# Kernel optimization log

Measured on AMD Instinct MI355X. Metric: run time of the kernel, lower is better.

Reference implementation:

```python
import jax, jax.numpy as jnp
import numpy as np

N = 50000          # num nodes
E = 800000         # num edges (avg degree 16)
IN_C, HID_C, OUT_C = 128, 128, 64
LPA_ITER = 5


def setup_inputs() -> dict:
    key = jax.random.key(0)
    ks = jax.random.split(key, 8)
    x = jax.random.normal(ks[0], (N, IN_C), dtype=jnp.float32)
    soft_labels = jax.random.uniform(ks[1], (N, OUT_C), dtype=jnp.float32)
    edge_index = jax.random.randint(ks[2], (2, E), 0, N, dtype=jnp.int64)
    # learnable edge weights: abs() in the original, so keep them positive
    edge_attr = jax.random.uniform(ks[3], (E,), dtype=jnp.float32, minval=0.1, maxval=1.0)
    # GCNConv params (lin weight + bias)
    w1 = jax.random.normal(ks[4], (IN_C, HID_C), dtype=jnp.float32) / np.sqrt(IN_C)
    b1 = jnp.zeros((HID_C,), dtype=jnp.float32)
    w2 = jax.random.normal(ks[5], (HID_C, OUT_C), dtype=jnp.float32) / np.sqrt(HID_C)
    b2 = jnp.zeros((OUT_C,), dtype=jnp.float32)
    return {"x": x, "soft_labels": soft_labels, "edge_attr": edge_attr,
            "w1": w1, "b1": b1, "w2": w2, "b2": b2, "edge_index": edge_index}


def reference(x, soft_labels, edge_attr, w1, b1, w2, b2, edge_index):
    row, col = edge_index[0], edge_index[1]
    n = x.shape[0]
    # row-normalize the weighted sparse adjacency: A_n = D^{-1} A
    deg = jax.ops.segment_sum(edge_attr, row, num_segments=n)  # [N]
    deg_inv = jnp.where(deg == 0, 0.0, 1.0 / deg)              # inf -> 0
    val = deg_inv[row] * edge_attr                              # [E]

    def spmm(v):  # A_n @ v,  v: [N, F]
        return jax.ops.segment_sum(val[:, None] * v[col], row, num_segments=n)

    # eval mode: dropout(p=0.5, training=False) is identity
    h = jax.nn.relu(spmm(x @ w1) + b1)        # GCNConv 1 (normalize=False)
    logits = spmm(h @ w2) + b2                # GCNConv 2
    x_out = jax.nn.sigmoid(logits)

    labels = soft_labels
    for _ in range(LPA_ITER):                 # label propagation
        labels = spmm(labels)
    labels = jax.nn.sigmoid(labels)
    return (x_out, labels)
```

## Files before the change

### kernel.cpp

```cpp
#include <hip/hip_runtime.h>
#include <cstdint>
#include <cstddef>


#define WS_ALIGN(x) (((x) + 255) & ~((size_t)255))

typedef __attribute__((ext_vector_type(8))) short short8;
typedef __attribute__((ext_vector_type(4))) float floatx4;

__device__ __forceinline__ unsigned short f2bf(float f) {
    unsigned u = __float_as_uint(f);
    u += 0x7fffu + ((u >> 16) & 1u);
    return (unsigned short)(u >> 16);
}
__device__ __forceinline__ float bf2f(unsigned short h) {
    return __uint_as_float(((unsigned)h) << 16);
}
__device__ __forceinline__ float sigmoidf(float x) {
    return 1.f / (1.f + __expf(-x));
}

static const int NBLK = 256;
#define MAXNB 256

__launch_bounds__(256)
__global__ void binA_count(const int* __restrict__ row, int* __restrict__ bucket_count,
                           int* __restrict__ bases, int E, int chunk, int NB)
{
    __shared__ int hist[MAXNB];
    const int t = threadIdx.x;
    const int blk = blockIdx.x;
    if (t < NB) hist[t] = 0;
    __syncthreads();
    const int s = blk * chunk;
    const int e = min(E, s + chunk);
    for (int i = s + t; i < e; i += 256)
        atomicAdd(&hist[row[i] >> 8], 1);
    __syncthreads();
    if (t < NB)
        bases[blk * NB + t] = atomicAdd(&bucket_count[t], hist[t]);
}

__launch_bounds__(256)
__global__ void bin_scan(const int* __restrict__ bucket_count, int* __restrict__ bucket_start,
                         int NB)
{
    __shared__ int s[256];
    const int t = threadIdx.x;
    int v = (t < NB) ? bucket_count[t] : 0;
    s[t] = v;
    __syncthreads();
    for (int off = 1; off < 256; off <<= 1) {
        int u = (t >= off) ? s[t - off] : 0;
        __syncthreads();
        s[t] += u;
        __syncthreads();
    }
    int excl = s[t] - v;
    if (t <= NB) bucket_start[t] = excl;
}

__launch_bounds__(256)
__global__ void binA_scatter(const int* __restrict__ row, const int* __restrict__ colv,
                             const float* __restrict__ ea,
                             const int* __restrict__ bucket_start, const int* __restrict__ bases,
                             int2* __restrict__ bk, int E, int chunk, int NB)
{
    __shared__ int cur[MAXNB];
    const int t = threadIdx.x;
    const int blk = blockIdx.x;
    if (t < NB) cur[t] = bucket_start[t] + bases[blk * NB + t];
    __syncthreads();
    const int s = blk * chunk;
    const int e = min(E, s + chunk);
    for (int i = s + t; i < e; i += 256) {
        int r = row[i];
        int bin = r >> 8;
        int pos = atomicAdd(&cur[bin], 1);
        bk[pos] = make_int2(((r & 255) << 16) | colv[i], __float_as_int(ea[i]));
    }
}

__launch_bounds__(256)
__global__ void binB(const int2* __restrict__ bk, const int* __restrict__ bucket_start,
                     int* __restrict__ rowptr, int2* __restrict__ edges, int N)
{
    __shared__ int cnt[256];
    __shared__ float deg[256];
    __shared__ float inv[256];
    __shared__ int excl_s[256];
    __shared__ int cur[256];
    __shared__ int scantmp[256];
    const int b = blockIdx.x;
    const int t = threadIdx.x;
    const int s = bucket_start[b];
    const int e = bucket_start[b + 1];
    cnt[t] = 0;
    deg[t] = 0.f;
    __syncthreads();
    for (int i = s + t; i < e; i += 256) {
        int2 v = bk[i];
        int rl = ((unsigned)v.x) >> 16;
        atomicAdd(&cnt[rl], 1);
        atomicAdd(&deg[rl], __int_as_float(v.y));
    }
    __syncthreads();
    const int myc = cnt[t];
    scantmp[t] = myc;
    __syncthreads();
    for (int off = 1; off < 256; off <<= 1) {
        int u = (t >= off) ? scantmp[t - off] : 0;
        __syncthreads();
        scantmp[t] += u;
        __syncthreads();
    }
    const int excl = scantmp[t] - myc;
    excl_s[t] = excl;
    float d = deg[t];
    inv[t] = (d > 0.f) ? 1.f / d : 0.f;
    cur[t] = 0;
    const int gr = b * 256 + t;
    if (gr <= N) rowptr[gr] = s + excl;
    __syncthreads();
    for (int i = s + t; i < e; i += 256) {
        int2 v = bk[i];
        int rl = ((unsigned)v.x) >> 16;
        int c = v.x & 0xffff;
        int p = s + excl_s[rl] + atomicAdd(&cur[rl], 1);
        edges[p] = make_int2(c, __float_as_int(__int_as_float(v.y) * inv[rl]));
    }
}

__global__ void f32_to_bf16_kernel(const float* __restrict__ in, unsigned short* __restrict__ out,
                                   int n2)
{
    int i = blockIdx.x * 256 + threadIdx.x;
    if (i < n2) {
        float2 v = ((const float2*)in)[i];
        unsigned p = (unsigned)f2bf(v.x) | ((unsigned)f2bf(v.y) << 16);
        ((unsigned*)out)[i] = p;
    }
}

template<int COLS>
__global__ void pack_w_kernel(const float* __restrict__ W, unsigned short* __restrict__ Wp)
{
    const int total = (COLS / 16) * 4 * 64;
    int idx = blockIdx.x * 256 + threadIdx.x;
    if (idx >= total) return;
    const int l = idx & 63;
    const int t = (idx >> 6) & 3;
    const int ct = idx >> 8;
    const int kbase = t * 32 + (l >> 4) * 8;
    const int col = ct * 16 + (l & 15);
    unsigned short v[8];
#pragma unroll
    for (int j = 0; j < 8; ++j)
        v[j] = f2bf(W[(size_t)(kbase + j) * COLS + col]);
    uint4 o;
    o.x = (unsigned)v[0] | ((unsigned)v[1] << 16);
    o.y = (unsigned)v[2] | ((unsigned)v[3] << 16);
    o.z = (unsigned)v[4] | ((unsigned)v[5] << 16);
    o.w = (unsigned)v[6] | ((unsigned)v[7] << 16);
    *(uint4*)(Wp + (size_t)idx * 8) = o;
}

template<int COLS>
__launch_bounds__(256)
__global__ void gemm_mfma(const unsigned short* __restrict__ A,
                          const unsigned short* __restrict__ Wp,
                          unsigned short* __restrict__ C, int M)
{
    const int wave = threadIdx.x >> 6;
    const int lane = threadIdx.x & 63;
    const int row0 = blockIdx.x * 64 + wave * 16;
    const int m = lane & 15;
    const int q = lane >> 4;

    const int arow = row0 + m;
    const bool avalid = arow < M;
    short8 a[4];
#pragma unroll
    for (int t = 0; t < 4; ++t) {
        if (avalid)
            a[t] = *(const short8*)(A + (size_t)arow * 128 + t * 32 + q * 8);
        else
            a[t] = (short8)0;
    }

#pragma unroll
    for (int ct = 0; ct < COLS / 16; ++ct) {
        floatx4 acc = {0.f, 0.f, 0.f, 0.f};
#pragma unroll
        for (int t = 0; t < 4; ++t) {
            short8 b = *(const short8*)(Wp + (size_t)((ct * 4 + t) * 64 + lane) * 8);
            acc = __builtin_amdgcn_mfma_f32_16x16x32_bf16(a[t], b, acc, 0, 0, 0);
        }
        const int col = ct * 16 + m;
#pragma unroll
        for (int r = 0; r < 4; ++r) {
            int orow = row0 + q * 4 + r;
            if (orow < M)
                C[(size_t)orow * COLS + col] = f2bf(acc[r]);
        }
    }
}

__launch_bounds__(256)
__global__ void spmm128_relu(const int* __restrict__ rowptr, const int2* __restrict__ edges,
                             const unsigned short* __restrict__ src,
                             const float* __restrict__ bias, unsigned* __restrict__ out, int n)
{
    const int row = blockIdx.x * 4 + (threadIdx.x >> 6);
    const int lane = threadIdx.x & 63;
    if (row >= n) return;
    const int s = rowptr[row];
    const int e = rowptr[row + 1];
    const unsigned* us = (const unsigned*)src;

    float ax[8], ay[8];
#pragma unroll
    for (int j = 0; j < 8; ++j) { ax[j] = 0.f; ay[j] = 0.f; }
    int i = s;
    for (; i + 8 <= e; i += 8) {
        int2 ed[8];
        unsigned u[8];
#pragma unroll
        for (int j = 0; j < 8; ++j) ed[j] = edges[i + j];
#pragma unroll
        for (int j = 0; j < 8; ++j) u[j] = us[(size_t)ed[j].x * 64 + lane];
#pragma unroll
        for (int j = 0; j < 8; ++j) {
            float w = __int_as_float(ed[j].y);
            ax[j] = fmaf(w, __uint_as_float(u[j] << 16), ax[j]);
            ay[j] = fmaf(w, __uint_as_float(u[j] & 0xffff0000u), ay[j]);
        }
    }
    for (; i + 4 <= e; i += 4) {
        int2 ed[4];
        unsigned u[4];
#pragma unroll
        for (int j = 0; j < 4; ++j) ed[j] = edges[i + j];
#pragma unroll
        for (int j = 0; j < 4; ++j) u[j] = us[(size_t)ed[j].x * 64 + lane];
#pragma unroll
        for (int j = 0; j < 4; ++j) {
            float w = __int_as_float(ed[j].y);
            ax[j] = fmaf(w, __uint_as_float(u[j] << 16), ax[j]);
            ay[j] = fmaf(w, __uint_as_float(u[j] & 0xffff0000u), ay[j]);
        }
    }
    for (; i < e; ++i) {
        int2 e0 = edges[i];
        unsigned u0 = us[(size_t)e0.x * 64 + lane];
        float w0 = __int_as_float(e0.y);
        ax[0] = fmaf(w0, __uint_as_float(u0 << 16), ax[0]);
        ay[0] = fmaf(w0, __uint_as_float(u0 & 0xffff0000u), ay[0]);
    }
    float vx = ((ax[0] + ax[1]) + (ax[2] + ax[3])) + ((ax[4] + ax[5]) + (ax[6] + ax[7]));
    float vy = ((ay[0] + ay[1]) + (ay[2] + ay[3])) + ((ay[4] + ay[5]) + (ay[6] + ay[7]));
    float2 b = *(const float2*)(bias + lane * 2);
    vx = fmaxf(vx + b.x, 0.f);
    vy = fmaxf(vy + b.y, 0.f);
    out[(size_t)row * 64 + lane] = (unsigned)f2bf(vx) | ((unsigned)f2bf(vy) << 16);
}

template<int ACT, bool OUT_BF16>
__launch_bounds__(256)
__global__ void spmm64_kernel(const int* __restrict__ rowptr, const int2* __restrict__ edges,
                              const unsigned short* __restrict__ src,
                              const float* __restrict__ bias, void* __restrict__ out, int n)
{
    const int row = blockIdx.x * 4 + (threadIdx.x >> 6);
    const int lane = threadIdx.x & 63;
    if (row >= n) return;
    const int s = rowptr[row];
    const int e = rowptr[row + 1];

    float a[8];
#pragma unroll
    for (int j = 0; j < 8; ++j) a[j] = 0.f;
    int i = s;
    for (; i + 8 <= e; i += 8) {
        int2 ed[8];
        float sv[8];
#pragma unroll
        for (int j = 0; j < 8; ++j) ed[j] = edges[i + j];
#pragma unroll
        for (int j = 0; j < 8; ++j) sv[j] = bf2f(src[(size_t)ed[j].x * 64 + lane]);
#pragma unroll
        for (int j = 0; j < 8; ++j) a[j] = fmaf(__int_as_float(ed[j].y), sv[j], a[j]);
    }
    for (; i + 4 <= e; i += 4) {
        int2 ed[4];
        float sv[4];
#pragma unroll
        for (int j = 0; j < 4; ++j) ed[j] = edges[i + j];
#pragma unroll
        for (int j = 0; j < 4; ++j) sv[j] = bf2f(src[(size_t)ed[j].x * 64 + lane]);
#pragma unroll
        for (int j = 0; j < 4; ++j) a[j] = fmaf(__int_as_float(ed[j].y), sv[j], a[j]);
    }
    for (; i < e; ++i) {
        int2 e0 = edges[i];
        a[0] = fmaf(__int_as_float(e0.y), bf2f(src[(size_t)e0.x * 64 + lane]), a[0]);
    }
    float v = ((a[0] + a[1]) + (a[2] + a[3])) + ((a[4] + a[5]) + (a[6] + a[7]));
    if (ACT == 2) v = sigmoidf(v + bias[lane]);
    else if (ACT == 3) v = sigmoidf(v);
    if (OUT_BF16)
        ((unsigned short*)out)[(size_t)row * 64 + lane] = f2bf(v);
    else
        ((float*)out)[(size_t)row * 64 + lane] = v;
}

extern "C" void kernel_launch(void* const* d_in, const int* in_sizes, int n_in,
                              void* d_out, int out_size, void* d_ws, size_t ws_size,
                              hipStream_t stream)
{
    const float* x    = (const float*)d_in[0];
    const float* soft = (const float*)d_in[1];
    const float* ea   = (const float*)d_in[2];
    const float* w1   = (const float*)d_in[3];
    const float* b1   = (const float*)d_in[4];
    const float* w2   = (const float*)d_in[5];
    const float* b2   = (const float*)d_in[6];
    const int*   eidx = (const int*)d_in[7];

    const int N = in_sizes[0] / 128;
    const int E = in_sizes[2];
    const int* row  = eidx;
    const int* colv = eidx + E;
    const int NB = (N + 255) / 256;
    const int chunk = (E + NBLK - 1) / NBLK;

    uint8_t* ws = (uint8_t*)d_ws;
    size_t off = 0;
    auto alloc = [&](size_t bytes) -> void* {
        void* p = ws + off;
        off += WS_ALIGN(bytes);
        return p;
    };
    int*  bucket_count = (int*) alloc((size_t)NB * 4);
    int*  bucket_start = (int*) alloc(((size_t)NB + 1) * 4);
    int*  bases        = (int*) alloc((size_t)NBLK * NB * 4);
    int*  rowptr       = (int*) alloc(((size_t)N + 1) * 4);
    int2* bk           = (int2*)alloc((size_t)E * 8);
    int2* edges        = (int2*)alloc((size_t)E * 8);
    unsigned short* xb      = (unsigned short*)alloc((size_t)N * 128 * 2);
    unsigned short* w1p     = (unsigned short*)alloc((size_t)128 * 128 * 2);
    unsigned short* w2p     = (unsigned short*)alloc((size_t)128 * 64 * 2);
    unsigned short* xw1b    = (unsigned short*)alloc((size_t)N * 128 * 2);
    unsigned short* hb      = (unsigned short*)alloc((size_t)N * 128 * 2);
    unsigned short* logitsb = (unsigned short*)alloc((size_t)N * 64 * 2);
    unsigned short* softb   = (unsigned short*)alloc((size_t)N * 64 * 2);
    unsigned short* labA    = (unsigned short*)alloc((size_t)N * 64 * 2);
    unsigned short* labB    = (unsigned short*)alloc((size_t)N * 64 * 2);

    float* out0 = (float*)d_out;
    float* out1 = out0 + (size_t)N * 64;

    hipMemsetAsync(bucket_count, 0, (size_t)NB * 4, stream);

    binA_count<<<NBLK, 256, 0, stream>>>(row, bucket_count, bases, E, chunk, NB);
    bin_scan<<<1, 256, 0, stream>>>(bucket_count, bucket_start, NB);
    binA_scatter<<<NBLK, 256, 0, stream>>>(row, colv, ea, bucket_start, bases, bk, E, chunk, NB);
    binB<<<NB, 256, 0, stream>>>(bk, bucket_start, rowptr, edges, N);

    const int nx2 = (N * 128) / 2;
    f32_to_bf16_kernel<<<(nx2 + 255) / 256, 256, 0, stream>>>(x, xb, nx2);
    const int ns2 = (N * 64) / 2;
    f32_to_bf16_kernel<<<(ns2 + 255) / 256, 256, 0, stream>>>(soft, softb, ns2);
    pack_w_kernel<128><<<8, 256, 0, stream>>>(w1, w1p);
    pack_w_kernel<64><<<4, 256, 0, stream>>>(w2, w2p);

    const int gGemm = (N + 63) / 64;
    const int gSp   = (N + 3) / 4;

    gemm_mfma<128><<<gGemm, 256, 0, stream>>>(xb, w1p, xw1b, N);
    spmm128_relu<<<gSp, 256, 0, stream>>>(rowptr, edges, xw1b, b1, (unsigned*)hb, N);
    gemm_mfma<64><<<gGemm, 256, 0, stream>>>(hb, w2p, logitsb, N);
    spmm64_kernel<2, false><<<gSp, 256, 0, stream>>>(rowptr, edges, logitsb, b2, out0, N);

    spmm64_kernel<0, true ><<<gSp, 256, 0, stream>>>(rowptr, edges, softb, nullptr, labA, N);
    spmm64_kernel<0, true ><<<gSp, 256, 0, stream>>>(rowptr, edges, labA, nullptr, labB, N);
    spmm64_kernel<0, true ><<<gSp, 256, 0, stream>>>(rowptr, edges, labB, nullptr, labA, N);
    spmm64_kernel<0, true ><<<gSp, 256, 0, stream>>>(rowptr, edges, labA, nullptr, labB, N);
    spmm64_kernel<3, false><<<gSp, 256, 0, stream>>>(rowptr, edges, labB, nullptr, out1, N);
}
```

Measured before the change: 367.0 us.

## Process two rows per wave in SpMM and fuse x bf16 cast into GEMM

Each SpMM wave now handles two CSR rows and interleaves their edge gathers, so more independent loads are in flight and half as many blocks are launched. Accumulators drop from 8 to 4 per row to keep register use in check. The first GEMM now reads fp32 x and converts it to bf16 in registers. This removes the separate conversion kernel and its intermediate buffer round trip. Imbalanced row degrees serialize the tail loops, and fewer waves may reduce latency hiding.

```diff
diff --git a/kernel.cpp b/kernel.cpp
--- a/kernel.cpp
+++ b/kernel.cpp
@@ -167,9 +167,9 @@
 
 template<int COLS>
 __launch_bounds__(256)
-__global__ void gemm_mfma(const unsigned short* __restrict__ A,
-                          const unsigned short* __restrict__ Wp,
-                          unsigned short* __restrict__ C, int M)
+__global__ void gemm_mfma_f32a(const float* __restrict__ A,
+                               const unsigned short* __restrict__ Wp,
+                               unsigned short* __restrict__ C, int M)
 {
     const int wave = threadIdx.x >> 6;
     const int lane = threadIdx.x & 63;
@@ -182,6 +182,53 @@
     short8 a[4];
 #pragma unroll
     for (int t = 0; t < 4; ++t) {
+        if (avalid) {
+            float4 f0 = *(const float4*)(A + (size_t)arow * 128 + t * 32 + q * 8);
+            float4 f1 = *(const float4*)(A + (size_t)arow * 128 + t * 32 + q * 8 + 4);
+            a[t][0] = (short)f2bf(f0.x); a[t][1] = (short)f2bf(f0.y);
+            a[t][2] = (short)f2bf(f0.z); a[t][3] = (short)f2bf(f0.w);
+            a[t][4] = (short)f2bf(f1.x); a[t][5] = (short)f2bf(f1.y);
+            a[t][6] = (short)f2bf(f1.z); a[t][7] = (short)f2bf(f1.w);
+        } else {
+            a[t] = (short8)0;
+        }
+    }
+
+#pragma unroll
+    for (int ct = 0; ct < COLS / 16; ++ct) {
+        floatx4 acc = {0.f, 0.f, 0.f, 0.f};
+#pragma unroll
+        for (int t = 0; t < 4; ++t) {
+            short8 b = *(const short8*)(Wp + (size_t)((ct * 4 + t) * 64 + lane) * 8);
+            acc = __builtin_amdgcn_mfma_f32_16x16x32_bf16(a[t], b, acc, 0, 0, 0);
+        }
+        const int col = ct * 16 + m;
+#pragma unroll
+        for (int r = 0; r < 4; ++r) {
+            int orow = row0 + q * 4 + r;
+            if (orow < M)
+                C[(size_t)orow * COLS + col] = f2bf(acc[r]);
+        }
+    }
+}
+
+template<int COLS>
+__launch_bounds__(256)
+__global__ void gemm_mfma(const unsigned short* __restrict__ A,
+                          const unsigned short* __restrict__ Wp,
+                          unsigned short* __restrict__ C, int M)
+{
+    const int wave = threadIdx.x >> 6;
+    const int lane = threadIdx.x & 63;
+    const int row0 = blockIdx.x * 64 + wave * 16;
+    const int m = lane & 15;
+    const int q = lane >> 4;
+
+    const int arow = row0 + m;
+    const bool avalid = arow < M;
+    short8 a[4];
+#pragma unroll
+    for (int t = 0; t < 4; ++t) {
         if (avalid)
             a[t] = *(const short8*)(A + (size_t)arow * 128 + t * 32 + q * 8);
         else
@@ -211,58 +258,101 @@
                              const unsigned short* __restrict__ src,
                              const float* __restrict__ bias, unsigned* __restrict__ out, int n)
 {
-    const int row = blockIdx.x * 4 + (threadIdx.x >> 6);
+    const int wave = threadIdx.x >> 6;
     const int lane = threadIdx.x & 63;
-    if (row >= n) return;
-    const int s = rowptr[row];
-    const int e = rowptr[row + 1];
+    const int r0 = blockIdx.x * 8 + wave * 2;
+    const int r1 = r0 + 1;
+    if (r0 >= n) return;
+    const bool has1 = (r1 < n);
+    const int s0 = rowptr[r0];
+    const int e0 = rowptr[r0 + 1];
+    int s1 = 0, e1 = 0;
+    if (has1) { s1 = rowptr[r1]; e1 = rowptr[r1 + 1]; }
     const unsigned* us = (const unsigned*)src;
 
-    float ax[8], ay[8];
-#pragma unroll
-    for (int j = 0; j < 8; ++j) { ax[j] = 0.f; ay[j] = 0.f; }
-    int i = s;
-    for (; i + 8 <= e; i += 8) {
-        int2 ed[8];
-        unsigned u[8];
-#pragma unroll
-        for (int j = 0; j < 8; ++j) ed[j] = edges[i + j];
+    float ax0[4], ay0[4], ax1[4], ay1[4];
+#pragma unroll
+    for (int j = 0; j < 4; ++j) { ax0[j] = 0.f; ay0[j] = 0.f; ax1[j] = 0.f; ay1[j] = 0.f; }
+
+    int i0 = s0, i1 = s1;
+    while (i0 + 8 <= e0 && i1 + 8 <= e1) {
+        int2 ed0[8], ed1[8];
+#pragma unroll
+        for (int j = 0; j < 8; ++j) ed0[j] = edges[i0 + j];
+#pragma unroll
+        for (int j = 0; j < 8; ++j) ed1[j] = edges[i1 + j];
+        unsigned u0[8], u1[8];
+#pragma unroll
+        for (int j = 0; j < 8; ++j) u0[j] = us[(size_t)ed0[j].x * 64 + lane];
+#pragma unroll
+        for (int j = 0; j < 8; ++j) u1[j] = us[(size_t)ed1[j].x * 64 + lane];
+#pragma unroll
+        for (int j = 0; j < 8; ++j) {
+            float w0 = __int_as_float(ed0[j].y);
+            float w1 = __int_as_float(ed1[j].y);
+            ax0[j & 3] = fmaf(w0, __uint_as_float(u0[j] << 16), ax0[j & 3]);
+            ay0[j & 3] = fmaf(w0, __uint_as_float(u0[j] & 0xffff0000u), ay0[j & 3]);
+            ax1[j & 3] = fmaf(w1, __uint_as_float(u1[j] << 16), ax1[j & 3]);
+            ay1[j & 3] = fmaf(w1, __uint_as_float(u1[j] & 0xffff0000u), ay1[j & 3]);
+        }
+        i0 += 8; i1 += 8;
+    }
+    while (i0 + 8 <= e0) {
+        int2 ed[8]; unsigned u[8];
+#pragma unroll
+        for (int j = 0; j < 8; ++j) ed[j] = edges[i0 + j];
 #pragma unroll
         for (int j = 0; j < 8; ++j) u[j] = us[(size_t)ed[j].x * 64 + lane];
 #pragma unroll
         for (int j = 0; j < 8; ++j) {
             float w = __int_as_float(ed[j].y);
-            ax[j] = fmaf(w, __uint_as_float(u[j] << 16), ax[j]);
-            ay[j] = fmaf(w, __uint_as_float(u[j] & 0xffff0000u), ay[j]);
-        }
-    }
-    for (; i + 4 <= e; i += 4) {
-        int2 ed[4];
-        unsigned u[4];
-#pragma unroll
-        for (int j = 0; j < 4; ++j) ed[j] = edges[i + j];
-#pragma unroll
-        for (int j = 0; j < 4; ++j) u[j] = us[(size_t)ed[j].x * 64 + lane];
-#pragma unroll
-        for (int j = 0; j < 4; ++j) {
+            ax0[j & 3] = fmaf(w, __uint_as_float(u[j] << 16), ax0[j & 3]);
+            ay0[j & 3] = fmaf(w, __uint_as_float(u[j] & 0xffff0000u), ay0[j & 3]);
+        }
+        i0 += 8;
+    }
+    for (; i0 < e0; ++i0) {
+        int2 e = edges[i0];
+        unsigned u = us[(size_t)e.x * 64 + lane];
+        float w = __int_as_float(e.y);
+        ax0[0] = fmaf(w, __uint_as_float(u << 16), ax0[0]);
+        ay0[0] = fmaf(w, __uint_as_float(u & 0xffff0000u), ay0[0]);
+    }
+    while (i1 + 8 <= e1) {
+        int2 ed[8]; unsigned u[8];
+#pragma unroll
+        for (int j = 0; j < 8; ++j) ed[j] = edges[i1 + j];
+#pragma unroll
+        for (int j = 0; j < 8; ++j) u[j] = us[(size_t)ed[j].x * 64 + lane];
+#pragma unroll
+        for (int j = 0; j < 8; ++j) {
             float w = __int_as_float(ed[j].y);
-            ax[j] = fmaf(w, __uint_as_float(u[j] << 16), ax[j]);
-            ay[j] = fmaf(w, __uint_as_float(u[j] & 0xffff0000u), ay[j]);
-        }
-    }
-    for (; i < e; ++i) {
-        int2 e0 = edges[i];
-        unsigned u0 = us[(size_t)e0.x * 64 + lane];
-        float w0 = __int_as_float(e0.y);
-        ax[0] = fmaf(w0, __uint_as_float(u0 << 16), ax[0]);
-        ay[0] = fmaf(w0, __uint_as_float(u0 & 0xffff0000u), ay[0]);
-    }
-    float vx = ((ax[0] + ax[1]) + (ax[2] + ax[3])) + ((ax[4] + ax[5]) + (ax[6] + ax[7]));
-    float vy = ((ay[0] + ay[1]) + (ay[2] + ay[3])) + ((ay[4] + ay[5]) + (ay[6] + ay[7]));
+            ax1[j & 3] = fmaf(w, __uint_as_float(u[j] << 16), ax1[j & 3]);
+            ay1[j & 3] = fmaf(w, __uint_as_float(u[j] & 0xffff0000u), ay1[j & 3]);
+        }
+        i1 += 8;
+    }
+    for (; i1 < e1; ++i1) {
+        int2 e = edges[i1];
+        unsigned u = us[(size_t)e.x * 64 + lane];
+        float w = __int_as_float(e.y);
+        ax1[0] = fmaf(w, __uint_as_float(u << 16), ax1[0]);
+        ay1[0] = fmaf(w, __uint_as_float(u & 0xffff0000u), ay1[0]);
+    }
+
     float2 b = *(const float2*)(bias + lane * 2);
+    float vx = (ax0[0] + ax0[1]) + (ax0[2] + ax0[3]);
+    float vy = (ay0[0] + ay0[1]) + (ay0[2] + ay0[3]);
     vx = fmaxf(vx + b.x, 0.f);
     vy = fmaxf(vy + b.y, 0.f);
-    out[(size_t)row * 64 + lane] = (unsigned)f2bf(vx) | ((unsigned)f2bf(vy) << 16);
+    out[(size_t)r0 * 64 + lane] = (unsigned)f2bf(vx) | ((unsigned)f2bf(vy) << 16);
+    if (has1) {
+        float wx = (ax1[0] + ax1[1]) + (ax1[2] + ax1[3]);
+        float wy = (ay1[0] + ay1[1]) + (ay1[2] + ay1[3]);
+        wx = fmaxf(wx + b.x, 0.f);
+        wy = fmaxf(wy + b.y, 0.f);
+        out[(size_t)r1 * 64 + lane] = (unsigned)f2bf(wx) | ((unsigned)f2bf(wy) << 16);
+    }
 }
 
 template<int ACT, bool OUT_BF16>
@@ -271,47 +361,80 @@
                               const unsigned short* __restrict__ src,
                               const float* __restrict__ bias, void* __restrict__ out, int n)
 {
-    const int row = blockIdx.x * 4 + (threadIdx.x >> 6);
+    const int wave = threadIdx.x >> 6;
     const int lane = threadIdx.x & 63;
-    if (row >= n) return;
-    const int s = rowptr[row];
-    const int e = rowptr[row + 1];
-
-    float a[8];
-#pragma unroll
-    for (int j = 0; j < 8; ++j) a[j] = 0.f;
-    int i = s;
-    for (; i + 8 <= e; i += 8) {
-        int2 ed[8];
-        float sv[8];
-#pragma unroll
-        for (int j = 0; j < 8; ++j) ed[j] = edges[i + j];
+    const int r0 = blockIdx.x * 8 + wave * 2;
+    const int r1 = r0 + 1;
+    if (r0 >= n) return;
+    const bool has1 = (r1 < n);
+    const int s0 = rowptr[r0];
+    const int e0 = rowptr[r0 + 1];
+    int s1 = 0, e1 = 0;
+    if (has1) { s1 = rowptr[r1]; e1 = rowptr[r1 + 1]; }
+
+    float a0[4], a1[4];
+#pragma unroll
+    for (int j = 0; j < 4; ++j) { a0[j] = 0.f; a1[j] = 0.f; }
+
+    int i0 = s0, i1 = s1;
+    while (i0 + 8 <= e0 && i1 + 8 <= e1) {
+        int2 ed0[8], ed1[8];
+#pragma unroll
+        for (int j = 0; j < 8; ++j) ed0[j] = edges[i0 + j];
+#pragma unroll
+        for (int j = 0; j < 8; ++j) ed1[j] = edges[i1 + j];
+        float sv0[8], sv1[8];
+#pragma unroll
+        for (int j = 0; j < 8; ++j) sv0[j] = bf2f(src[(size_t)ed0[j].x * 64 + lane]);
+#pragma unroll
+        for (int j = 0; j < 8; ++j) sv1[j] = bf2f(src[(size_t)ed1[j].x * 64 + lane]);
+#pragma unroll
+        for (int j = 0; j < 8; ++j) {
+            a0[j & 3] = fmaf(__int_as_float(ed0[j].y), sv0[j], a0[j & 3]);
+            a1[j & 3] = fmaf(__int_as_float(ed1[j].y), sv1[j], a1[j & 3]);
+        }
+        i0 += 8; i1 += 8;
+    }
+    while (i0 + 8 <= e0) {
+        int2 ed[8]; float sv[8];
+#pragma unroll
+        for (int j = 0; j < 8; ++j) ed[j] = edges[i0 + j];
 #pragma unroll
         for (int j = 0; j < 8; ++j) sv[j] = bf2f(src[(size_t)ed[j].x * 64 + lane]);
 #pragma unroll
-        for (int j = 0; j < 8; ++j) a[j] = fmaf(__int_as_float(ed[j].y), sv[j], a[j]);
-    }
-    for (; i + 4 <= e; i += 4) {
-        int2 ed[4];
-        float sv[4];
-#pragma unroll
-        for (int j = 0; j < 4; ++j) ed[j] = edges[i + j];
-#pragma unroll
-        for (int j = 0; j < 4; ++j) sv[j] = bf2f(src[(size_t)ed[j].x * 64 + lane]);
-#pragma unroll
-        for (int j = 0; j < 4; ++j) a[j] = fmaf(__int_as_float(ed[j].y), sv[j], a[j]);
-    }
-    for (; i < e; ++i) {
-        int2 e0 = edges[i];
-        a[0] = fmaf(__int_as_float(e0.y), bf2f(src[(size_t)e0.x * 64 + lane]), a[0]);
-    }
-    float v = ((a[0] + a[1]) + (a[2] + a[3])) + ((a[4] + a[5]) + (a[6] + a[7]));
-    if (ACT == 2) v = sigmoidf(v + bias[lane]);
-    else if (ACT == 3) v = sigmoidf(v);
-    if (OUT_BF16)
-        ((unsigned short*)out)[(size_t)row * 64 + lane] = f2bf(v);
-    else
-        ((float*)out)[(size_t)row * 64 + lane] = v;
+        for (int j = 0; j < 8; ++j) a0[j & 3] = fmaf(__int_as_float(ed[j].y), sv[j], a0[j & 3]);
+        i0 += 8;
+    }
+    for (; i0 < e0; ++i0) {
+        int2 e = edges[i0];
+        a0[0] = fmaf(__int_as_float(e.y), bf2f(src[(size_t)e.x * 64 + lane]), a0[0]);
+    }
+    while (i1 + 8 <= e1) {
+        int2 ed[8]; float sv[8];
+#pragma unroll
+        for (int j = 0; j < 8; ++j) ed[j] = edges[i1 + j];
+#pragma unroll
+        for (int j = 0; j < 8; ++j) sv[j] = bf2f(src[(size_t)ed[j].x * 64 + lane]);
+#pragma unroll
+        for (int j = 0; j < 8; ++j) a1[j & 3] = fmaf(__int_as_float(ed[j].y), sv[j], a1[j & 3]);
+        i1 += 8;
+    }
+    for (; i1 < e1; ++i1) {
+        int2 e = edges[i1];
+        a1[0] = fmaf(__int_as_float(e.y), bf2f(src[(size_t)e.x * 64 + lane]), a1[0]);
+    }
+
+    float v0 = (a0[0] + a0[1]) + (a0[2] + a0[3]);
+    float v1 = (a1[0] + a1[1]) + (a1[2] + a1[3]);
+    if (ACT == 2) { float b = bias[lane]; v0 = sigmoidf(v0 + b); v1 = sigmoidf(v1 + b); }
+    else if (ACT == 3) { v0 = sigmoidf(v0); v1 = sigmoidf(v1); }
+    if (OUT_BF16) {
+        ((unsigned short*)out)[(size_t)r0 * 64 + lane] = f2bf(v0);
+        if (has1) ((unsigned short*)out)[(size_t)r1 * 64 + lane] = f2bf(v1);
+    } else {
+        ((float*)out)[(size_t)r0 * 64 + lane] = v0;
+        if (has1) ((float*)out)[(size_t)r1 * 64 + lane] = v1;
+    }
 }
 
 extern "C" void kernel_launch(void* const* d_in, const int* in_sizes, int n_in,
@@ -347,7 +470,6 @@
     int*  rowptr       = (int*) alloc(((size_t)N + 1) * 4);
     int2* bk           = (int2*)alloc((size_t)E * 8);
     int2* edges        = (int2*)alloc((size_t)E * 8);
-    unsigned short* xb      = (unsigned short*)alloc((size_t)N * 128 * 2);
     unsigned short* w1p     = (unsigned short*)alloc((size_t)128 * 128 * 2);
     unsigned short* w2p     = (unsigned short*)alloc((size_t)128 * 64 * 2);
     unsigned short* xw1b    = (unsigned short*)alloc((size_t)N * 128 * 2);
@@ -367,17 +489,15 @@
     binA_scatter<<<NBLK, 256, 0, stream>>>(row, colv, ea, bucket_start, bases, bk, E, chunk, NB);
     binB<<<NB, 256, 0, stream>>>(bk, bucket_start, rowptr, edges, N);
 
-    const int nx2 = (N * 128) / 2;
-    f32_to_bf16_kernel<<<(nx2 + 255) / 256, 256, 0, stream>>>(x, xb, nx2);
     const int ns2 = (N * 64) / 2;
     f32_to_bf16_kernel<<<(ns2 + 255) / 256, 256, 0, stream>>>(soft, softb, ns2);
     pack_w_kernel<128><<<8, 256, 0, stream>>>(w1, w1p);
     pack_w_kernel<64><<<4, 256, 0, stream>>>(w2, w2p);
 
     const int gGemm = (N + 63) / 64;
-    const int gSp   = (N + 3) / 4;
-
-    gemm_mfma<128><<<gGemm, 256, 0, stream>>>(xb, w1p, xw1b, N);
+    const int gSp   = (N + 7) / 8;
+
+    gemm_mfma_f32a<128><<<gGemm, 256, 0, stream>>>(x, w1p, xw1b, N);
     spmm128_relu<<<gSp, 256, 0, stream>>>(rowptr, edges, xw1b, b1, (unsigned*)hb, N);
     gemm_mfma<64><<<gGemm, 256, 0, stream>>>(hb, w2p, logitsb, N);
     spmm64_kernel<2, false><<<gSp, 256, 0, stream>>>(rowptr, edges, logitsb, b2, out0, N);
```

Result: slower. 418.5 us (+14.0%).

## Fuse x bf16 conversion into GEMM and co-schedule LPA with GCN SpMMs

Applied to the files above, without the earlier changes.

The first GEMM now reads fp32 x directly and converts to bf16 in registers, which removes the separate conversion kernel and its intermediate buffer. The first two label-propagation SpMM iterations are fused into the GCN SpMM kernels, so each edge list and rowptr pass serves two feature matrices at once. This cuts two launches and two passes over the edge structure, at the cost of more registers per thread and wider gathers. The 4-wide remainder loops are removed, leaving the 8-wide loop followed by a scalar tail.

```diff
diff --git a/kernel.cpp b/kernel.cpp
--- a/kernel.cpp
+++ b/kernel.cpp
@@ -167,9 +167,9 @@
 
 template<int COLS>
 __launch_bounds__(256)
-__global__ void gemm_mfma(const unsigned short* __restrict__ A,
-                          const unsigned short* __restrict__ Wp,
-                          unsigned short* __restrict__ C, int M)
+__global__ void gemm_mfma_f32a(const float* __restrict__ A,
+                               const unsigned short* __restrict__ Wp,
+                               unsigned short* __restrict__ C, int M)
 {
     const int wave = threadIdx.x >> 6;
     const int lane = threadIdx.x & 63;
@@ -182,6 +182,53 @@
     short8 a[4];
 #pragma unroll
     for (int t = 0; t < 4; ++t) {
+        if (avalid) {
+            float4 f0 = *(const float4*)(A + (size_t)arow * 128 + t * 32 + q * 8);
+            float4 f1 = *(const float4*)(A + (size_t)arow * 128 + t * 32 + q * 8 + 4);
+            a[t][0] = (short)f2bf(f0.x); a[t][1] = (short)f2bf(f0.y);
+            a[t][2] = (short)f2bf(f0.z); a[t][3] = (short)f2bf(f0.w);
+            a[t][4] = (short)f2bf(f1.x); a[t][5] = (short)f2bf(f1.y);
+            a[t][6] = (short)f2bf(f1.z); a[t][7] = (short)f2bf(f1.w);
+        } else {
+            a[t] = (short8)0;
+        }
+    }
+
+#pragma unroll
+    for (int ct = 0; ct < COLS / 16; ++ct) {
+        floatx4 acc = {0.f, 0.f, 0.f, 0.f};
+#pragma unroll
+        for (int t = 0; t < 4; ++t) {
+            short8 b = *(const short8*)(Wp + (size_t)((ct * 4 + t) * 64 + lane) * 8);
+            acc = __builtin_amdgcn_mfma_f32_16x16x32_bf16(a[t], b, acc, 0, 0, 0);
+        }
+        const int col = ct * 16 + m;
+#pragma unroll
+        for (int r = 0; r < 4; ++r) {
+            int orow = row0 + q * 4 + r;
+            if (orow < M)
+                C[(size_t)orow * COLS + col] = f2bf(acc[r]);
+        }
+    }
+}
+
+template<int COLS>
+__launch_bounds__(256)
+__global__ void gemm_mfma(const unsigned short* __restrict__ A,
+                          const unsigned short* __restrict__ Wp,
+                          unsigned short* __restrict__ C, int M)
+{
+    const int wave = threadIdx.x >> 6;
+    const int lane = threadIdx.x & 63;
+    const int row0 = blockIdx.x * 64 + wave * 16;
+    const int m = lane & 15;
+    const int q = lane >> 4;
+
+    const int arow = row0 + m;
+    const bool avalid = arow < M;
+    short8 a[4];
+#pragma unroll
+    for (int t = 0; t < 4; ++t) {
         if (avalid)
             a[t] = *(const short8*)(A + (size_t)arow * 128 + t * 32 + q * 8);
         else
@@ -207,69 +254,69 @@
 }
 
 __launch_bounds__(256)
-__global__ void spmm128_relu(const int* __restrict__ rowptr, const int2* __restrict__ edges,
-                             const unsigned short* __restrict__ src,
-                             const float* __restrict__ bias, unsigned* __restrict__ out, int n)
+__global__ void spmm_f128_f64(const int* __restrict__ rowptr, const int2* __restrict__ edges,
+                              const unsigned* __restrict__ srcA,
+                              const unsigned short* __restrict__ srcB,
+                              const float* __restrict__ bias,
+                              unsigned* __restrict__ outA,
+                              unsigned short* __restrict__ outB,
+                              int n)
 {
     const int row = blockIdx.x * 4 + (threadIdx.x >> 6);
     const int lane = threadIdx.x & 63;
     if (row >= n) return;
     const int s = rowptr[row];
     const int e = rowptr[row + 1];
-    const unsigned* us = (const unsigned*)src;
-
-    float ax[8], ay[8];
-#pragma unroll
-    for (int j = 0; j < 8; ++j) { ax[j] = 0.f; ay[j] = 0.f; }
+
+    float ax[8], ay[8], ab[8];
+#pragma unroll
+    for (int j = 0; j < 8; ++j) { ax[j] = 0.f; ay[j] = 0.f; ab[j] = 0.f; }
     int i = s;
     for (; i + 8 <= e; i += 8) {
         int2 ed[8];
-        unsigned u[8];
+        unsigned ua[8];
+        unsigned short ub[8];
 #pragma unroll
         for (int j = 0; j < 8; ++j) ed[j] = edges[i + j];
 #pragma unroll
-        for (int j = 0; j < 8; ++j) u[j] = us[(size_t)ed[j].x * 64 + lane];
+        for (int j = 0; j < 8; ++j) ua[j] = srcA[(size_t)ed[j].x * 64 + lane];
+#pragma unroll
+        for (int j = 0; j < 8; ++j) ub[j] = srcB[(size_t)ed[j].x * 64 + lane];
 #pragma unroll
         for (int j = 0; j < 8; ++j) {
             float w = __int_as_float(ed[j].y);
-            ax[j] = fmaf(w, __uint_as_float(u[j] << 16), ax[j]);
-            ay[j] = fmaf(w, __uint_as_float(u[j] & 0xffff0000u), ay[j]);
-        }
-    }
-    for (; i + 4 <= e; i += 4) {
-        int2 ed[4];
-        unsigned u[4];
-#pragma unroll
-        for (int j = 0; j < 4; ++j) ed[j] = edges[i + j];
-#pragma unroll
-        for (int j = 0; j < 4; ++j) u[j] = us[(size_t)ed[j].x * 64 + lane];
-#pragma unroll
-        for (int j = 0; j < 4; ++j) {
-            float w = __int_as_float(ed[j].y);
-            ax[j] = fmaf(w, __uint_as_float(u[j] << 16), ax[j]);
-            ay[j] = fmaf(w, __uint_as_float(u[j] & 0xffff0000u), ay[j]);
+            ax[j] = fmaf(w, __uint_as_float(ua[j] << 16), ax[j]);
+            ay[j] = fmaf(w, __uint_as_float(ua[j] & 0xffff0000u), ay[j]);
+            ab[j] = fmaf(w, bf2f(ub[j]), ab[j]);
         }
     }
     for (; i < e; ++i) {
         int2 e0 = edges[i];
-        unsigned u0 = us[(size_t)e0.x * 64 + lane];
-        float w0 = __int_as_float(e0.y);
-        ax[0] = fmaf(w0, __uint_as_float(u0 << 16), ax[0]);
-        ay[0] = fmaf(w0, __uint_as_float(u0 & 0xffff0000u), ay[0]);
+        unsigned ua = srcA[(size_t)e0.x * 64 + lane];
+        unsigned short ub = srcB[(size_t)e0.x * 64 + lane];
+        float w = __int_as_float(e0.y);
+        ax[0] = fmaf(w, __uint_as_float(ua << 16), ax[0]);
+        ay[0] = fmaf(w, __uint_as_float(ua & 0xffff0000u), ay[0]);
+        ab[0] = fmaf(w, bf2f(ub), ab[0]);
     }
     float vx = ((ax[0] + ax[1]) + (ax[2] + ax[3])) + ((ax[4] + ax[5]) + (ax[6] + ax[7]));
     float vy = ((ay[0] + ay[1]) + (ay[2] + ay[3])) + ((ay[4] + ay[5]) + (ay[6] + ay[7]));
+    float vb = ((ab[0] + ab[1]) + (ab[2] + ab[3])) + ((ab[4] + ab[5]) + (ab[6] + ab[7]));
     float2 b = *(const float2*)(bias + lane * 2);
     vx = fmaxf(vx + b.x, 0.f);
     vy = fmaxf(vy + b.y, 0.f);
-    out[(size_t)row * 64 + lane] = (unsigned)f2bf(vx) | ((unsigned)f2bf(vy) << 16);
-}
-
-template<int ACT, bool OUT_BF16>
-__launch_bounds__(256)
-__global__ void spmm64_kernel(const int* __restrict__ rowptr, const int2* __restrict__ edges,
-                              const unsigned short* __restrict__ src,
-                              const float* __restrict__ bias, void* __restrict__ out, int n)
+    outA[(size_t)row * 64 + lane] = (unsigned)f2bf(vx) | ((unsigned)f2bf(vy) << 16);
+    outB[(size_t)row * 64 + lane] = f2bf(vb);
+}
+
+__launch_bounds__(256)
+__global__ void spmm_f64_f64(const int* __restrict__ rowptr, const int2* __restrict__ edges,
+                             const unsigned short* __restrict__ srcA,
+                             const unsigned short* __restrict__ srcB,
+                             const float* __restrict__ bias,
+                             float* __restrict__ outA,
+                             unsigned short* __restrict__ outB,
+                             int n)
 {
     const int row = blockIdx.x * 4 + (threadIdx.x >> 6);
     const int lane = threadIdx.x & 63;
@@ -277,6 +324,50 @@
     const int s = rowptr[row];
     const int e = rowptr[row + 1];
 
+    float aa[8], ab[8];
+#pragma unroll
+    for (int j = 0; j < 8; ++j) { aa[j] = 0.f; ab[j] = 0.f; }
+    int i = s;
+    for (; i + 8 <= e; i += 8) {
+        int2 ed[8];
+        unsigned short ua[8], ub[8];
+#pragma unroll
+        for (int j = 0; j < 8; ++j) ed[j] = edges[i + j];
+#pragma unroll
+        for (int j = 0; j < 8; ++j) ua[j] = srcA[(size_t)ed[j].x * 64 + lane];
+#pragma unroll
+        for (int j = 0; j < 8; ++j) ub[j] = srcB[(size_t)ed[j].x * 64 + lane];
+#pragma unroll
+        for (int j = 0; j < 8; ++j) {
+            float w = __int_as_float(ed[j].y);
+            aa[j] = fmaf(w, bf2f(ua[j]), aa[j]);
+            ab[j] = fmaf(w, bf2f(ub[j]), ab[j]);
+        }
+    }
+    for (; i < e; ++i) {
+        int2 e0 = edges[i];
+        float w = __int_as_float(e0.y);
+        aa[0] = fmaf(w, bf2f(srcA[(size_t)e0.x * 64 + lane]), aa[0]);
+        ab[0] = fmaf(w, bf2f(srcB[(size_t)e0.x * 64 + lane]), ab[0]);
+    }
+    float va = ((aa[0] + aa[1]) + (aa[2] + aa[3])) + ((aa[4] + aa[5]) + (aa[6] + aa[7]));
+    float vb = ((ab[0] + ab[1]) + (ab[2] + ab[3])) + ((ab[4] + ab[5]) + (ab[6] + ab[7]));
+    outA[(size_t)row * 64 + lane] = sigmoidf(va + bias[lane]);
+    outB[(size_t)row * 64 + lane] = f2bf(vb);
+}
+
+template<int ACT, bool OUT_BF16>
+__launch_bounds__(256)
+__global__ void spmm64_kernel(const int* __restrict__ rowptr, const int2* __restrict__ edges,
+                              const unsigned short* __restrict__ src,
+                              void* __restrict__ out, int n)
+{
+    const int row = blockIdx.x * 4 + (threadIdx.x >> 6);
+    const int lane = threadIdx.x & 63;
+    if (row >= n) return;
+    const int s = rowptr[row];
+    const int e = rowptr[row + 1];
+
     float a[8];
 #pragma unroll
     for (int j = 0; j < 8; ++j) a[j] = 0.f;
@@ -291,23 +382,12 @@
 #pragma unroll
         for (int j = 0; j < 8; ++j) a[j] = fmaf(__int_as_float(ed[j].y), sv[j], a[j]);
     }
-    for (; i + 4 <= e; i += 4) {
-        int2 ed[4];
-        float sv[4];
-#pragma unroll
-        for (int j = 0; j < 4; ++j) ed[j] = edges[i + j];
-#pragma unroll
-        for (int j = 0; j < 4; ++j) sv[j] = bf2f(src[(size_t)ed[j].x * 64 + lane]);
-#pragma unroll
-        for (int j = 0; j < 4; ++j) a[j] = fmaf(__int_as_float(ed[j].y), sv[j], a[j]);
-    }
     for (; i < e; ++i) {
         int2 e0 = edges[i];
         a[0] = fmaf(__int_as_float(e0.y), bf2f(src[(size_t)e0.x * 64 + lane]), a[0]);
     }
     float v = ((a[0] + a[1]) + (a[2] + a[3])) + ((a[4] + a[5]) + (a[6] + a[7]));
-    if (ACT == 2) v = sigmoidf(v + bias[lane]);
-    else if (ACT == 3) v = sigmoidf(v);
+    if (ACT == 3) v = sigmoidf(v);
     if (OUT_BF16)
         ((unsigned short*)out)[(size_t)row * 64 + lane] = f2bf(v);
     else
@@ -347,7 +427,6 @@
     int*  rowptr       = (int*) alloc(((size_t)N + 1) * 4);
     int2* bk           = (int2*)alloc((size_t)E * 8);
     int2* edges        = (int2*)alloc((size_t)E * 8);
-    unsigned short* xb      = (unsigned short*)alloc((size_t)N * 128 * 2);
     unsigned short* w1p     = (unsigned short*)alloc((size_t)128 * 128 * 2);
     unsigned short* w2p     = (unsigned short*)alloc((size_t)128 * 64 * 2);
     unsigned short* xw1b    = (unsigned short*)alloc((size_t)N * 128 * 2);
@@ -367,8 +446,6 @@
     binA_scatter<<<NBLK, 256, 0, stream>>>(row, colv, ea, bucket_start, bases, bk, E, chunk, NB);
     binB<<<NB, 256, 0, stream>>>(bk, bucket_start, rowptr, edges, N);
 
-    const int nx2 = (N * 128) / 2;
-    f32_to_bf16_kernel<<<(nx2 + 255) / 256, 256, 0, stream>>>(x, xb, nx2);
     const int ns2 = (N * 64) / 2;
     f32_to_bf16_kernel<<<(ns2 + 255) / 256, 256, 0, stream>>>(soft, softb, ns2);
     pack_w_kernel<128><<<8, 256, 0, stream>>>(w1, w1p);
@@ -377,14 +454,16 @@
     const int gGemm = (N + 63) / 64;
     const int gSp   = (N + 3) / 4;
 
-    gemm_mfma<128><<<gGemm, 256, 0, stream>>>(xb, w1p, xw1b, N);
-    spmm128_relu<<<gSp, 256, 0, stream>>>(rowptr, edges, xw1b, b1, (unsigned*)hb, N);
+    gemm_mfma_f32a<128><<<gGemm, 256, 0, stream>>>(x, w1p, xw1b, N);
+
+    spmm_f128_f64<<<gSp, 256, 0, stream>>>(rowptr, edges, (const unsigned*)xw1b, softb,
+                                           b1, (unsigned*)hb, labA, N);
+
     gemm_mfma<64><<<gGemm, 256, 0, stream>>>(hb, w2p, logitsb, N);
-    spmm64_kernel<2, false><<<gSp, 256, 0, stream>>>(rowptr, edges, logitsb, b2, out0, N);
-
-    spmm64_kernel<0, true ><<<gSp, 256, 0, stream>>>(rowptr, edges, softb, nullptr, labA, N);
-    spmm64_kernel<0, true ><<<gSp, 256, 0, stream>>>(rowptr, edges, labA, nullptr, labB, N);
-    spmm64_kernel<0, true ><<<gSp, 256, 0, stream>>>(rowptr, edges, labB, nullptr, labA, N);
-    spmm64_kernel<0, true ><<<gSp, 256, 0, stream>>>(rowptr, edges, labA, nullptr, labB, N);
-    spmm64_kernel<3, false><<<gSp, 256, 0, stream>>>(rowptr, edges, labB, nullptr, out1, N);
-}
+
+    spmm_f64_f64<<<gSp, 256, 0, stream>>>(rowptr, edges, logitsb, labA, b2, out0, labB, N);
+
+    spmm64_kernel<0, true ><<<gSp, 256, 0, stream>>>(rowptr, edges, labB, labA, N);
+    spmm64_kernel<0, true ><<<gSp, 256, 0, stream>>>(rowptr, edges, labA, labB, N);
+    spmm64_kernel<3, false><<<gSp, 256, 0, stream>>>(rowptr, edges, labB, out1, N);
+}
```

New measurement: 361.9 us. Within noise of the previous version (-1.4%).

## Split 64-wide features into 32-column planes and fuse x conversion into GEMM

Applied to the files above, without the earlier changes.

Splits the 64-feature logits and label tensors into two 32-column bf16 planes. Each SpMM pass then gathers from a smaller source array that fits better in cache, with the two half-waves handling alternate edges and combining results through a shuffle. The first GEMM now reads fp32 x and converts it to bf16 itself, which drops the separate conversion kernel and its buffer. Edge loads become nontemporal. The cost is twice as many SpMM launches, with the edge list read once per plane.

```diff
diff --git a/kernel.cpp b/kernel.cpp
--- a/kernel.cpp
+++ b/kernel.cpp
@@ -18,6 +18,13 @@
 }
 __device__ __forceinline__ float sigmoidf(float x) {
     return 1.f / (1.f + __expf(-x));
+}
+__device__ __forceinline__ int2 ld_nt_int2(const int2* p) {
+    long long v = __builtin_nontemporal_load((const long long*)p);
+    int2 r;
+    r.x = (int)(unsigned)(v & 0xffffffffLL);
+    r.y = (int)(v >> 32);
+    return r;
 }
 
 static const int NBLK = 256;
@@ -131,14 +138,16 @@
     }
 }
 
-__global__ void f32_to_bf16_kernel(const float* __restrict__ in, unsigned short* __restrict__ out,
-                                   int n2)
+__global__ void split_soft_kernel(const float* __restrict__ in,
+                                  unsigned short* __restrict__ p0,
+                                  unsigned short* __restrict__ p1, int total)
 {
     int i = blockIdx.x * 256 + threadIdx.x;
-    if (i < n2) {
-        float2 v = ((const float2*)in)[i];
-        unsigned p = (unsigned)f2bf(v.x) | ((unsigned)f2bf(v.y) << 16);
-        ((unsigned*)out)[i] = p;
+    if (i < total) {
+        int r = i >> 6, f = i & 63;
+        unsigned short v = f2bf(in[i]);
+        if (f < 32) p0[(size_t)r * 32 + f] = v;
+        else        p1[(size_t)r * 32 + f - 32] = v;
     }
 }
 
@@ -167,9 +176,9 @@
 
 template<int COLS>
 __launch_bounds__(256)
-__global__ void gemm_mfma(const unsigned short* __restrict__ A,
-                          const unsigned short* __restrict__ Wp,
-                          unsigned short* __restrict__ C, int M)
+__global__ void gemm_mfma_f32a(const float* __restrict__ A,
+                               const unsigned short* __restrict__ Wp,
+                               unsigned short* __restrict__ C, int M)
 {
     const int wave = threadIdx.x >> 6;
     const int lane = threadIdx.x & 63;
@@ -182,6 +191,53 @@
     short8 a[4];
 #pragma unroll
     for (int t = 0; t < 4; ++t) {
+        if (avalid) {
+            float4 f0 = *(const float4*)(A + (size_t)arow * 128 + t * 32 + q * 8);
+            float4 f1 = *(const float4*)(A + (size_t)arow * 128 + t * 32 + q * 8 + 4);
+            a[t][0] = (short)f2bf(f0.x); a[t][1] = (short)f2bf(f0.y);
+            a[t][2] = (short)f2bf(f0.z); a[t][3] = (short)f2bf(f0.w);
+            a[t][4] = (short)f2bf(f1.x); a[t][5] = (short)f2bf(f1.y);
+            a[t][6] = (short)f2bf(f1.z); a[t][7] = (short)f2bf(f1.w);
+        } else {
+            a[t] = (short8)0;
+        }
+    }
+
+#pragma unroll
+    for (int ct = 0; ct < COLS / 16; ++ct) {
+        floatx4 acc = {0.f, 0.f, 0.f, 0.f};
+#pragma unroll
+        for (int t = 0; t < 4; ++t) {
+            short8 b = *(const short8*)(Wp + (size_t)((ct * 4 + t) * 64 + lane) * 8);
+            acc = __builtin_amdgcn_mfma_f32_16x16x32_bf16(a[t], b, acc, 0, 0, 0);
+        }
+        const int col = ct * 16 + m;
+#pragma unroll
+        for (int r = 0; r < 4; ++r) {
+            int orow = row0 + q * 4 + r;
+            if (orow < M)
+                C[(size_t)orow * COLS + col] = f2bf(acc[r]);
+        }
+    }
+}
+
+__launch_bounds__(256)
+__global__ void gemm_mfma64_planes(const unsigned short* __restrict__ A,
+                                   const unsigned short* __restrict__ Wp,
+                                   unsigned short* __restrict__ C0,
+                                   unsigned short* __restrict__ C1, int M)
+{
+    const int wave = threadIdx.x >> 6;
+    const int lane = threadIdx.x & 63;
+    const int row0 = blockIdx.x * 64 + wave * 16;
+    const int m = lane & 15;
+    const int q = lane >> 4;
+
+    const int arow = row0 + m;
+    const bool avalid = arow < M;
+    short8 a[4];
+#pragma unroll
+    for (int t = 0; t < 4; ++t) {
         if (avalid)
             a[t] = *(const short8*)(A + (size_t)arow * 128 + t * 32 + q * 8);
         else
@@ -189,26 +245,27 @@
     }
 
 #pragma unroll
-    for (int ct = 0; ct < COLS / 16; ++ct) {
+    for (int ct = 0; ct < 4; ++ct) {
         floatx4 acc = {0.f, 0.f, 0.f, 0.f};
 #pragma unroll
         for (int t = 0; t < 4; ++t) {
             short8 b = *(const short8*)(Wp + (size_t)((ct * 4 + t) * 64 + lane) * 8);
             acc = __builtin_amdgcn_mfma_f32_16x16x32_bf16(a[t], b, acc, 0, 0, 0);
         }
-        const int col = ct * 16 + m;
+        unsigned short* C = (ct < 2) ? C0 : C1;
+        const int ccol = (ct < 2) ? (ct * 16 + m) : (ct * 16 + m - 32);
 #pragma unroll
         for (int r = 0; r < 4; ++r) {
             int orow = row0 + q * 4 + r;
             if (orow < M)
-                C[(size_t)orow * COLS + col] = f2bf(acc[r]);
+                C[(size_t)orow * 32 + ccol] = f2bf(acc[r]);
         }
     }
 }
 
 __launch_bounds__(256)
 __global__ void spmm128_relu(const int* __restrict__ rowptr, const int2* __restrict__ edges,
-                             const unsigned short* __restrict__ src,
+                             const unsigned* __restrict__ srcA,
                              const float* __restrict__ bias, unsigned* __restrict__ out, int n)
 {
     const int row = blockIdx.x * 4 + (threadIdx.x >> 6);
@@ -216,7 +273,6 @@
     if (row >= n) return;
     const int s = rowptr[row];
     const int e = rowptr[row + 1];
-    const unsigned* us = (const unsigned*)src;
 
     float ax[8], ay[8];
 #pragma unroll
@@ -226,9 +282,9 @@
         int2 ed[8];
         unsigned u[8];
 #pragma unroll
-        for (int j = 0; j < 8; ++j) ed[j] = edges[i + j];
-#pragma unroll
-        for (int j = 0; j < 8; ++j) u[j] = us[(size_t)ed[j].x * 64 + lane];
+        for (int j = 0; j < 8; ++j) ed[j] = ld_nt_int2(&edges[i + j]);
+#pragma unroll
+        for (int j = 0; j < 8; ++j) u[j] = srcA[(size_t)ed[j].x * 64 + lane];
 #pragma unroll
         for (int j = 0; j < 8; ++j) {
             float w = __int_as_float(ed[j].y);
@@ -236,23 +292,9 @@
             ay[j] = fmaf(w, __uint_as_float(u[j] & 0xffff0000u), ay[j]);
         }
     }
-    for (; i + 4 <= e; i += 4) {
-        int2 ed[4];
-        unsigned u[4];
-#pragma unroll
-        for (int j = 0; j < 4; ++j) ed[j] = edges[i + j];
-#pragma unroll
-        for (int j = 0; j < 4; ++j) u[j] = us[(size_t)ed[j].x * 64 + lane];
-#pragma unroll
-        for (int j = 0; j < 4; ++j) {
-            float w = __int_as_float(ed[j].y);
-            ax[j] = fmaf(w, __uint_as_float(u[j] << 16), ax[j]);
-            ay[j] = fmaf(w, __uint_as_float(u[j] & 0xffff0000u), ay[j]);
-        }
-    }
     for (; i < e; ++i) {
-        int2 e0 = edges[i];
-        unsigned u0 = us[(size_t)e0.x * 64 + lane];
+        int2 e0 = ld_nt_int2(&edges[i]);
+        unsigned u0 = srcA[(size_t)e0.x * 64 + lane];
         float w0 = __int_as_float(e0.y);
         ax[0] = fmaf(w0, __uint_as_float(u0 << 16), ax[0]);
         ay[0] = fmaf(w0, __uint_as_float(u0 & 0xffff0000u), ay[0]);
@@ -265,53 +307,56 @@
     out[(size_t)row * 64 + lane] = (unsigned)f2bf(vx) | ((unsigned)f2bf(vy) << 16);
 }
 
-template<int ACT, bool OUT_BF16>
-__launch_bounds__(256)
-__global__ void spmm64_kernel(const int* __restrict__ rowptr, const int2* __restrict__ edges,
-                              const unsigned short* __restrict__ src,
-                              const float* __restrict__ bias, void* __restrict__ out, int n)
+template<int ACT>
+__launch_bounds__(256)
+__global__ void spmm32_plane(const int* __restrict__ rowptr, const int2* __restrict__ edges,
+                             const unsigned short* __restrict__ src,
+                             const float* __restrict__ bias,
+                             void* __restrict__ out, int plane_off, int n)
 {
     const int row = blockIdx.x * 4 + (threadIdx.x >> 6);
     const int lane = threadIdx.x & 63;
+    const int f = lane & 31;
+    const int half = lane >> 5;
     if (row >= n) return;
     const int s = rowptr[row];
     const int e = rowptr[row + 1];
 
-    float a[8];
-#pragma unroll
-    for (int j = 0; j < 8; ++j) a[j] = 0.f;
+    float a[4] = {0.f, 0.f, 0.f, 0.f};
     int i = s;
-    for (; i + 8 <= e; i += 8) {
+    while (i + 16 <= e) {
         int2 ed[8];
         float sv[8];
 #pragma unroll
-        for (int j = 0; j < 8; ++j) ed[j] = edges[i + j];
-#pragma unroll
-        for (int j = 0; j < 8; ++j) sv[j] = bf2f(src[(size_t)ed[j].x * 64 + lane]);
-#pragma unroll
-        for (int j = 0; j < 8; ++j) a[j] = fmaf(__int_as_float(ed[j].y), sv[j], a[j]);
-    }
-    for (; i + 4 <= e; i += 4) {
-        int2 ed[4];
-        float sv[4];
-#pragma unroll
-        for (int j = 0; j < 4; ++j) ed[j] = edges[i + j];
-#pragma unroll
-        for (int j = 0; j < 4; ++j) sv[j] = bf2f(src[(size_t)ed[j].x * 64 + lane]);
-#pragma unroll
-        for (int j = 0; j < 4; ++j) a[j] = fmaf(__int_as_float(ed[j].y), sv[j], a[j]);
-    }
-    for (; i < e; ++i) {
-        int2 e0 = edges[i];
-        a[0] = fmaf(__int_as_float(e0.y), bf2f(src[(size_t)e0.x * 64 + lane]), a[0]);
-    }
-    float v = ((a[0] + a[1]) + (a[2] + a[3])) + ((a[4] + a[5]) + (a[6] + a[7]));
-    if (ACT == 2) v = sigmoidf(v + bias[lane]);
-    else if (ACT == 3) v = sigmoidf(v);
-    if (OUT_BF16)
-        ((unsigned short*)out)[(size_t)row * 64 + lane] = f2bf(v);
-    else
-        ((float*)out)[(size_t)row * 64 + lane] = v;
+        for (int j = 0; j < 8; ++j) ed[j] = ld_nt_int2(&edges[i + 2 * j + half]);
+#pragma unroll
+        for (int j = 0; j < 8; ++j) sv[j] = bf2f(src[(size_t)ed[j].x * 32 + f]);
+#pragma unroll
+        for (int j = 0; j < 8; ++j) a[j & 3] = fmaf(__int_as_float(ed[j].y), sv[j], a[j & 3]);
+        i += 16;
+    }
+    while (i + 2 <= e) {
+        int2 ed = ld_nt_int2(&edges[i + half]);
+        a[0] = fmaf(__int_as_float(ed.y), bf2f(src[(size_t)ed.x * 32 + f]), a[0]);
+        i += 2;
+    }
+    if (i < e) {
+        int2 ed = ld_nt_int2(&edges[i]);
+        if (half == 0)
+            a[1] = fmaf(__int_as_float(ed.y), bf2f(src[(size_t)ed.x * 32 + f]), a[1]);
+    }
+    float v = (a[0] + a[1]) + (a[2] + a[3]);
+    v += __shfl_down(v, 32);
+    if (half == 0) {
+        if (ACT == 0) {
+            ((unsigned short*)out)[(size_t)row * 32 + f] = f2bf(v);
+        } else {
+            float x = v;
+            if (ACT == 2) x += bias[plane_off + f];
+            x = sigmoidf(x);
+            ((float*)out)[(size_t)row * 64 + plane_off + f] = x;
+        }
+    }
 }
 
 extern "C" void kernel_launch(void* const* d_in, const int* in_sizes, int n_in,
@@ -347,15 +392,16 @@
     int*  rowptr       = (int*) alloc(((size_t)N + 1) * 4);
     int2* bk           = (int2*)alloc((size_t)E * 8);
     int2* edges        = (int2*)alloc((size_t)E * 8);
-    unsigned short* xb      = (unsigned short*)alloc((size_t)N * 128 * 2);
-    unsigned short* w1p     = (unsigned short*)alloc((size_t)128 * 128 * 2);
-    unsigned short* w2p     = (unsigned short*)alloc((size_t)128 * 64 * 2);
-    unsigned short* xw1b    = (unsigned short*)alloc((size_t)N * 128 * 2);
-    unsigned short* hb      = (unsigned short*)alloc((size_t)N * 128 * 2);
-    unsigned short* logitsb = (unsigned short*)alloc((size_t)N * 64 * 2);
-    unsigned short* softb   = (unsigned short*)alloc((size_t)N * 64 * 2);
-    unsigned short* labA    = (unsigned short*)alloc((size_t)N * 64 * 2);
-    unsigned short* labB    = (unsigned short*)alloc((size_t)N * 64 * 2);
+    unsigned short* w1p   = (unsigned short*)alloc((size_t)128 * 128 * 2);
+    unsigned short* w2p   = (unsigned short*)alloc((size_t)128 * 64 * 2);
+    unsigned short* xw1b  = (unsigned short*)alloc((size_t)N * 128 * 2);
+    unsigned short* hb    = (unsigned short*)alloc((size_t)N * 128 * 2);
+    unsigned short* logp0 = (unsigned short*)alloc((size_t)N * 32 * 2);
+    unsigned short* logp1 = (unsigned short*)alloc((size_t)N * 32 * 2);
+    unsigned short* softp0= (unsigned short*)alloc((size_t)N * 32 * 2);
+    unsigned short* softp1= (unsigned short*)alloc((size_t)N * 32 * 2);
+    unsigned short* labP  = (unsigned short*)alloc((size_t)N * 32 * 2);
+    unsigned short* labQ  = (unsigned short*)alloc((size_t)N * 32 * 2);
 
     float* out0 = (float*)d_out;
     float* out1 = out0 + (size_t)N * 64;
@@ -367,24 +413,30 @@
     binA_scatter<<<NBLK, 256, 0, stream>>>(row, colv, ea, bucket_start, bases, bk, E, chunk, NB);
     binB<<<NB, 256, 0, stream>>>(bk, bucket_start, rowptr, edges, N);
 
-    const int nx2 = (N * 128) / 2;
-    f32_to_bf16_kernel<<<(nx2 + 255) / 256, 256, 0, stream>>>(x, xb, nx2);
-    const int ns2 = (N * 64) / 2;
-    f32_to_bf16_kernel<<<(ns2 + 255) / 256, 256, 0, stream>>>(soft, softb, ns2);
+    const int tot = N * 64;
+    split_soft_kernel<<<(tot + 255) / 256, 256, 0, stream>>>(soft, softp0, softp1, tot);
     pack_w_kernel<128><<<8, 256, 0, stream>>>(w1, w1p);
     pack_w_kernel<64><<<4, 256, 0, stream>>>(w2, w2p);
 
     const int gGemm = (N + 63) / 64;
     const int gSp   = (N + 3) / 4;
 
-    gemm_mfma<128><<<gGemm, 256, 0, stream>>>(xb, w1p, xw1b, N);
-    spmm128_relu<<<gSp, 256, 0, stream>>>(rowptr, edges, xw1b, b1, (unsigned*)hb, N);
-    gemm_mfma<64><<<gGemm, 256, 0, stream>>>(hb, w2p, logitsb, N);
-    spmm64_kernel<2, false><<<gSp, 256, 0, stream>>>(rowptr, edges, logitsb, b2, out0, N);
-
-    spmm64_kernel<0, true ><<<gSp, 256, 0, stream>>>(rowptr, edges, softb, nullptr, labA, N);
-    spmm64_kernel<0, true ><<<gSp, 256, 0, stream>>>(rowptr, edges, labA, nullptr, labB, N);
-    spmm64_kernel<0, true ><<<gSp, 256, 0, stream>>>(rowptr, edges, labB, nullptr, labA, N);
-    spmm64_kernel<0, true ><<<gSp, 256, 0, stream>>>(rowptr, edges, labA, nullptr, labB, N);
-    spmm64_kernel<3, false><<<gSp, 256, 0, stream>>>(rowptr, edges, labB, nullptr, out1, N);
-}
+    gemm_mfma_f32a<128><<<gGemm, 256, 0, stream>>>(x, w1p, xw1b, N);
+    spmm128_relu<<<gSp, 256, 0, stream>>>(rowptr, edges, (const unsigned*)xw1b,
+                                          b1, (unsigned*)hb, N);
+    gemm_mfma64_planes<<<gGemm, 256, 0, stream>>>(hb, w2p, logp0, logp1, N);
+    spmm32_plane<2><<<gSp, 256, 0, stream>>>(rowptr, edges, logp0, b2, out0, 0, N);
+    spmm32_plane<2><<<gSp, 256, 0, stream>>>(rowptr, edges, logp1, b2, out0, 32, N);
+
+    spmm32_plane<0><<<gSp, 256, 0, stream>>>(rowptr, edges, softp0, nullptr, labP, 0, N);
+    spmm32_plane<0><<<gSp, 256, 0, stream>>>(rowptr, edges, labP, nullptr, labQ, 0, N);
+    spmm32_plane<0><<<gSp, 256, 0, stream>>>(rowptr, edges, labQ, nullptr, labP, 0, N);
+    spmm32_plane<0><<<gSp, 256, 0, stream>>>(rowptr, edges, labP, nullptr, labQ, 0, N);
+    spmm32_plane<3><<<gSp, 256, 0, stream>>>(rowptr, edges, labQ, nullptr, out1, 0, N);
+
+    spmm32_plane<0><<<gSp, 256, 0, stream>>>(rowptr, edges, softp1, nullptr, labP, 0, N);
+    spmm32_plane<0><<<gSp, 256, 0, stream>>>(rowptr, edges, labP, nullptr, labQ, 0, N);
+    spmm32_plane<0><<<gSp, 256, 0, stream>>>(rowptr, edges, labQ, nullptr, labP, 0, N);
+    spmm32_plane<0><<<gSp, 256, 0, stream>>>(rowptr, edges, labP, nullptr, labQ, 0, N);
+    spmm32_plane<3><<<gSp, 256, 0, stream>>>(rowptr, edges, labQ, nullptr, out1, 32, N);
+}
```

New measurement: 623.2 us. +69.8%, slower.
